# Performance work log

Measured on AMD Instinct MI355X. Metric: run time of the kernel, lower is better.

Reference implementation:

```python
import jax, jax.numpy as jnp
import numpy as np

N = 40000          # nodes
E = 320000         # edges
IN_DIM = 16
H = 64             # num_hidden
EDGE_DIM = 8
NUM_FILTERS = 2
SCALE = 3
T = 4              # num_layers (time steps)
DC = EDGE_DIM * NUM_FILTERS   # edge_dim_cat = 16
HC = H + DC                   # concat(h, efeat_p) dim
S1 = SCALE - 1


def setup_inputs() -> dict:
    key = jax.random.key(0)
    ks = jax.random.split(key, 24)
    def nrm(k, shape, fan):
        return jax.random.normal(k, shape, dtype=jnp.float32) / np.float32(np.sqrt(fan))
    return {
        "inputs": jax.random.normal(ks[0], (N, IN_DIM), dtype=jnp.float32),
        "e_feats": jax.random.normal(ks[1], (E, EDGE_DIM, T), dtype=jnp.float32),
        "rain0": jax.random.uniform(ks[2], (N, T), dtype=jnp.float32),
        "src": jax.random.randint(ks[3], (E,), 0, N),
        "dst": jax.random.randint(ks[4], (E,), 0, N),
        # embedding (no bias)
        "W_emb": nrm(ks[5], (IN_DIM, H), IN_DIM),
        # ST_EIConvSPGRAD (IN) layers, one per scale step: edge MLP split into per-source terms
        "Win_hs": nrm(ks[6], (S1, H, H), 2 * H + EDGE_DIM + 1),
        "Win_hd": nrm(ks[7], (S1, H, H), 2 * H + EDGE_DIM + 1),
        "Win_e": nrm(ks[8], (S1, EDGE_DIM, H), 2 * H + EDGE_DIM + 1),
        "Win_r": nrm(ks[9], (S1, H), 2 * H + EDGE_DIM + 1),
        # ST_EIConvProp (PROP) layers (edge-feature propagation, out_on=False)
        "Wp_hs": nrm(ks[10], (S1, H, DC), 2 * H + DC + 1),
        "Wp_hd": nrm(ks[11], (S1, H, DC), 2 * H + DC + 1),
        "Wp_e": nrm(ks[12], (S1, DC, DC), 2 * H + DC + 1),
        "Wp_r": nrm(ks[13], (S1, DC), 2 * H + DC + 1),
        # ST_EIConvProp OUT layer (out_on=True) on concatenated node features
        "Wo_hs": nrm(ks[14], (HC, H), 2 * HC + EDGE_DIM + 1),
        "Wo_hd": nrm(ks[15], (HC, H), 2 * HC + EDGE_DIM + 1),
        "Wo_e": nrm(ks[16], (EDGE_DIM, H), 2 * HC + EDGE_DIM + 1),
        "Wo_r": nrm(ks[17], (H,), 2 * HC + EDGE_DIM + 1),
        "W_rain": nrm(ks[18], (H,), H),
    }


def reference(inputs, e_feats, rain0, src, dst,
              W_emb, Win_hs, Win_hd, Win_e, Win_r,
              Wp_hs, Wp_hd, Wp_e, Wp_r,
              Wo_hs, Wo_hd, Wo_e, Wo_r, W_rain):
    relu = jax.nn.relu
    agg = lambda m: jax.ops.segment_sum(m, dst, num_segments=N)

    def in_layer(s, h, ef, rain):
        # per-edge message: MLP over [h_src, h_dst, efeat, rain_src], split matmuls avoid concat
        m = relu(h[src] @ Win_hs[s] + h[dst] @ Win_hd[s]
                 + ef @ Win_e[s] + rain[src, None] * Win_r[s][None, :])
        return relu(agg(m))                      # [N, H]

    def prop_layer(s, h, ef, rain):
        # ef is edge-level [E, DC] on first call, node-level [N, DC] thereafter (gather at src)
        ef_e = ef if ef.shape[0] == E else ef[src]
        m = relu(h[src] @ Wp_hs[s] + h[dst] @ Wp_hd[s]
                 + ef_e @ Wp_e[s] + rain[src, None] * Wp_r[s][None, :])
        return agg(m)                            # [N, DC]

    def out_layer(h_out, ef, rain):
        m = relu(h_out[src] @ Wo_hs + h_out[dst] @ Wo_hd
                 + ef @ Wo_e + rain[src, None] * Wo_r[None, :])
        h_new = relu(agg(m))                     # [N, H]
        rain_out = h_new @ W_rain                # [N]
        return rain_out, h_new

    def step(h, ef_t, rain_t, first):
        for s in range(S1):
            h = in_layer(s, h, ef_t, rain_t)
        ef_exp = jnp.tile(ef_t, (1, NUM_FILTERS))        # [E, DC]
        p = prop_layer(0, h, ef_exp, rain_t)
        # faithful quirk: first time step re-applies PROP[0] (range starts at 0);
        # later steps start at 1
        rng = range(S1) if first else range(1, S1)
        for s in rng:
            p = prop_layer(s, h, p, rain_t)
        h_out = jnp.concatenate([h, p], axis=1)          # [N, HC]
        rain_m, h = out_layer(h_out, ef_t, rain_t)
        return rain_m, h

    h = inputs @ W_emb                                   # [N, H]
    rains = []
    for t in range(T):
        rain_m, h = step(h, e_feats[:, :, t], rain0[:, t], first=(t == 0))
        rains.append(rain_m)
    return jnp.stack(rains, axis=1)                      # [N, T]
```

## Files before the change

kernel.cpp:

```cpp
#include <hip/hip_runtime.h>

#define NN 40000
#define NE 320000
#define TT 4
#define SCAN_CHUNK 1024
#define NBLK_SCAN ((NN + SCAN_CHUNK - 1) / SCAN_CHUNK)

typedef float vf4 __attribute__((ext_vector_type(4)));

__device__ __forceinline__ float bcastf(float v, int k) {
    return __builtin_bit_cast(float, __builtin_amdgcn_readlane(__builtin_bit_cast(int, v), k));
}
__device__ __forceinline__ int bcasti(int v, int k) {
    return __builtin_amdgcn_readlane(v, k);
}

__global__ void emb_kernel(const float* __restrict__ x, const float* __restrict__ W,
                           float* __restrict__ h) {
    int i = blockIdx.x * blockDim.x + threadIdx.x;
    if (i >= NN * 64) return;
    int n = i >> 6, j = i & 63;
    float acc = 0.f;
#pragma unroll
    for (int k = 0; k < 16; ++k) acc = fmaf(x[n * 16 + k], W[k * 64 + j], acc);
    h[i] = acc;
}

__global__ void wfold_kernel(const float* __restrict__ We, float* __restrict__ Wf) {
    int i = threadIdx.x;
    if (i < 128) Wf[i] = We[i] + We[i + 128];
}

__global__ void hist_kernel(const int* __restrict__ dst, int* __restrict__ deg) {
    int e = blockIdx.x * blockDim.x + threadIdx.x;
    if (e < NE) atomicAdd(&deg[dst[e]], 1);
}

__global__ void scan1_kernel(const int* __restrict__ deg, int* __restrict__ bsum) {
    __shared__ int sdata[256];
    int b = blockIdx.x, t = threadIdx.x;
    int base = b * SCAN_CHUNK;
    int sum = 0;
    for (int i = t; i < SCAN_CHUNK; i += 256) {
        int idx = base + i;
        sum += (idx < NN) ? deg[idx] : 0;
    }
    sdata[t] = sum;
    __syncthreads();
    for (int off = 128; off > 0; off >>= 1) {
        if (t < off) sdata[t] += sdata[t + off];
        __syncthreads();
    }
    if (t == 0) bsum[b] = sdata[0];
}

__global__ void scan2_kernel(const int* __restrict__ bsum, int* __restrict__ boff,
                             int* __restrict__ rowptr) {
    if (threadIdx.x == 0) {
        int acc = 0;
        for (int i = 0; i < NBLK_SCAN; ++i) {
            boff[i] = acc;
            acc += bsum[i];
        }
        rowptr[NN] = NE;
    }
}

__global__ void scan3_kernel(const int* __restrict__ deg, const int* __restrict__ boff,
                             int* __restrict__ rowptr) {
    __shared__ int ss[256];
    int b = blockIdx.x, t = threadIdx.x;
    int base = b * SCAN_CHUNK + t * 4;
    int v[4], s = 0;
#pragma unroll
    for (int q = 0; q < 4; ++q) {
        int idx = base + q;
        v[q] = (idx < NN) ? deg[idx] : 0;
        s += v[q];
    }
    ss[t] = s;
    __syncthreads();
    for (int off = 1; off < 256; off <<= 1) {
        int add = (t >= off) ? ss[t - off] : 0;
        __syncthreads();
        ss[t] += add;
        __syncthreads();
    }
    int excl = boff[b] + ss[t] - s;
#pragma unroll
    for (int q = 0; q < 4; ++q) {
        int idx = base + q;
        if (idx < NN) rowptr[idx] = excl;
        excl += v[q];
    }
}

__global__ void scatter_kernel(const int* __restrict__ src, const int* __restrict__ dst,
                               int* __restrict__ cursor, int* __restrict__ perm,
                               int* __restrict__ srcp) {
    int e = blockIdx.x * blockDim.x + threadIdx.x;
    if (e >= NE) return;
    int d = dst[e];
    int pos = atomicAdd(&cursor[d], 1);
    perm[pos] = e;
    srcp[pos] = src[e];
}

__global__ void efperm_all_kernel(const float* __restrict__ ef, const int* __restrict__ perm,
                                  float* __restrict__ out) {
    int pos = blockIdx.x * blockDim.x + threadIdx.x;
    if (pos >= NE) return;
    int e = perm[pos];
    const float4* e4 = reinterpret_cast<const float4*>(ef) + (size_t)e * 8;
#pragma unroll
    for (int k = 0; k < 8; ++k) {
        float4 v = e4[k];
        out[0 * (size_t)NE * 8 + pos * 8 + k] = v.x;
        out[1 * (size_t)NE * 8 + pos * 8 + k] = v.y;
        out[2 * (size_t)NE * 8 + pos * 8 + k] = v.z;
        out[3 * (size_t)NE * 8 + pos * 8 + k] = v.w;
    }
}

__global__ void efperm_one_kernel(const float* __restrict__ ef, const int* __restrict__ perm,
                                  int t, float* __restrict__ out) {
    int i = blockIdx.x * blockDim.x + threadIdx.x;
    if (i >= NE * 8) return;
    int pos = i >> 3, k = i & 7;
    int e = perm[pos];
    out[i] = ef[((size_t)e * 8 + k) * 4 + t];
}

__global__ __launch_bounds__(256) void node_ab_kernel(
    const float* __restrict__ X1, int relu1,
    const float* __restrict__ X2, int d2,
    const float* __restrict__ Whs, const float* __restrict__ Whd,
    const float* __restrict__ rain, const float* __restrict__ Wr,
    float* __restrict__ A, float* __restrict__ B) {
    extern __shared__ float sW[];
    const int dtot = 64 + d2;
    float* sWs = sW;
    float* sWd = sW + (dtot << 6);
    for (int i = threadIdx.x; i < (dtot << 6); i += 256) {
        sWs[i] = Whs[i];
        sWd[i] = Whd[i];
    }
    __syncthreads();
    const int lane = threadIdx.x & 63;
    const int wid = (blockIdx.x << 2) + (threadIdx.x >> 6);
    const int n0 = wid << 3;
    const float wr = Wr[lane];
    float xv[8], aa[8], bb[8];
#pragma unroll
    for (int p = 0; p < 8; ++p) {
        float x = __builtin_nontemporal_load(&X1[(n0 + p) * 64 + lane]);
        xv[p] = relu1 ? fmaxf(x, 0.f) : x;
        aa[p] = rain[(n0 + p) * TT] * wr;
        bb[p] = 0.f;
    }
#pragma unroll 16
    for (int k = 0; k < 64; ++k) {
        float ws = sWs[(k << 6) + lane];
        float wd = sWd[(k << 6) + lane];
#pragma unroll
        for (int p = 0; p < 8; ++p) {
            float xk = bcastf(xv[p], k);
            aa[p] = fmaf(xk, ws, aa[p]);
            bb[p] = fmaf(xk, wd, bb[p]);
        }
    }
    if (d2) {
#pragma unroll
        for (int p = 0; p < 8; ++p) xv[p] = X2[(n0 + p) * 16 + (lane & 15)];
#pragma unroll
        for (int k = 0; k < 16; ++k) {
            float ws = sWs[((64 + k) << 6) + lane];
            float wd = sWd[((64 + k) << 6) + lane];
#pragma unroll
            for (int p = 0; p < 8; ++p) {
                float xk = bcastf(xv[p], k);
                aa[p] = fmaf(xk, ws, aa[p]);
                bb[p] = fmaf(xk, wd, bb[p]);
            }
        }
    }
#pragma unroll
    for (int p = 0; p < 8; ++p) {
        A[(n0 + p) * 64 + lane] = aa[p];
        B[(n0 + p) * 64 + lane] = bb[p];
    }
}

__global__ __launch_bounds__(256) void node_p_kernel(
    const float* __restrict__ X, const float* __restrict__ P, int has_p,
    const float* __restrict__ Whs, const float* __restrict__ Whd,
    const float* __restrict__ We,
    const float* __restrict__ rain, const float* __restrict__ Wr,
    float* __restrict__ Ap, float* __restrict__ Bp) {
    __shared__ float sX[64 * 68];
    __shared__ float sP[64 * 20];
    __shared__ float sWs[1024], sWd[1024], sWe[256];
    for (int i = threadIdx.x; i < 1024; i += 256) {
        sWs[i] = Whs[i];
        sWd[i] = Whd[i];
    }
    sWe[threadIdx.x] = has_p ? We[threadIdx.x] : 0.f;
    const int n0 = blockIdx.x << 6;
    for (int i = threadIdx.x; i < 1024; i += 256) {
        int row = i >> 4, col = (i & 15) << 2;
        const float4 v = *reinterpret_cast<const float4*>(&X[(n0 + row) * 64 + col]);
        float* d = &sX[row * 68 + col];
        d[0] = fmaxf(v.x, 0.f);
        d[1] = fmaxf(v.y, 0.f);
        d[2] = fmaxf(v.z, 0.f);
        d[3] = fmaxf(v.w, 0.f);
    }
    if (has_p) {
        int row = threadIdx.x >> 2, col = (threadIdx.x & 3) << 2;
        const float4 v = *reinterpret_cast<const float4*>(&P[(n0 + row) * 16 + col]);
        float* d = &sP[row * 20 + col];
        d[0] = v.x; d[1] = v.y; d[2] = v.z; d[3] = v.w;
    }
    __syncthreads();
    const int j = threadIdx.x & 15;
    const int nl0 = threadIdx.x >> 4;
    const float wr = Wr[j];
    float a[4], b[4];
#pragma unroll
    for (int q = 0; q < 4; ++q) {
        int n = n0 + nl0 + (q << 4);
        a[q] = rain[n * TT] * wr;
        b[q] = 0.f;
    }
#pragma unroll 8
    for (int k = 0; k < 64; ++k) {
        float wa = sWs[(k << 4) + j];
        float wb = sWd[(k << 4) + j];
#pragma unroll
        for (int q = 0; q < 4; ++q) {
            float x = sX[(nl0 + (q << 4)) * 68 + k];
            a[q] = fmaf(x, wa, a[q]);
            b[q] = fmaf(x, wb, b[q]);
        }
    }
    if (has_p) {
#pragma unroll
        for (int k = 0; k < 16; ++k) {
            float wa = sWe[(k << 4) + j];
#pragma unroll
            for (int q = 0; q < 4; ++q) {
                float x = sP[(nl0 + (q << 4)) * 20 + k];
                a[q] = fmaf(x, wa, a[q]);
            }
        }
    }
#pragma unroll
    for (int q = 0; q < 4; ++q) {
        int n = n0 + nl0 + (q << 4);
        Ap[n * 16 + j] = a[q];
        Bp[n * 16 + j] = b[q];
    }
}

__global__ __launch_bounds__(256) void edge64_csr(
    const float* __restrict__ A, const float* __restrict__ B,
    const float* __restrict__ efp, const float* __restrict__ We,
    const int* __restrict__ rowptr, const int* __restrict__ srcp,
    float* __restrict__ agg, const float* __restrict__ Wrain,
    float* __restrict__ out, int t) {
    const int lane = threadIdx.x & 63;
    const int n = (blockIdx.x << 2) + (threadIdx.x >> 6);
    const float w0 = We[0 * 64 + lane], w1 = We[1 * 64 + lane];
    const float w2 = We[2 * 64 + lane], w3 = We[3 * 64 + lane];
    const float w4 = We[4 * 64 + lane], w5 = We[5 * 64 + lane];
    const float w6 = We[6 * 64 + lane], w7 = We[7 * 64 + lane];
    const int beg = rowptr[n], end = rowptr[n + 1];
    const int deg = end - beg;
    int sv = 0;
    if (beg + lane < NE) sv = srcp[beg + lane];
    const float b = __builtin_nontemporal_load(&B[(size_t)n * 64 + lane]);
    const vf4* ef4 = reinterpret_cast<const vf4*>(efp);
    float acc = 0.f;
    for (int k0 = 0; k0 < deg; k0 += 4) {
        float av[4];
        vf4 f0[4], f1[4];
#pragma unroll
        for (int i = 0; i < 4; ++i) {
            int kk = k0 + i;
            if (kk > deg - 1) kk = deg - 1;
            int s = (kk < 64) ? bcasti(sv, kk) : srcp[beg + kk];
            av[i] = A[(size_t)s * 64 + lane];
            f0[i] = ef4[(size_t)(beg + kk) * 2];
            f1[i] = ef4[(size_t)(beg + kk) * 2 + 1];
        }
#pragma unroll
        for (int i = 0; i < 4; ++i) {
            if (k0 + i < deg) {
                float m = av[i] + b;
                m = fmaf(f0[i].x, w0, m);
                m = fmaf(f0[i].y, w1, m);
                m = fmaf(f0[i].z, w2, m);
                m = fmaf(f0[i].w, w3, m);
                m = fmaf(f1[i].x, w4, m);
                m = fmaf(f1[i].y, w5, m);
                m = fmaf(f1[i].z, w6, m);
                m = fmaf(f1[i].w, w7, m);
                acc += fmaxf(m, 0.f);
            }
        }
    }
    __builtin_nontemporal_store(acc, &agg[(size_t)n * 64 + lane]);
    if (out) {
        float r = fmaxf(acc, 0.f) * Wrain[lane];
#pragma unroll
        for (int off = 32; off > 0; off >>= 1) r += __shfl_down(r, off);
        if (lane == 0) out[n * TT + t] = r;
    }
}

__global__ __launch_bounds__(256) void edge16_csr_ef(
    const float* __restrict__ Ap, const float* __restrict__ Bp,
    const float* __restrict__ efp, const float* __restrict__ Wf,
    const int* __restrict__ rowptr, const int* __restrict__ srcp,
    float* __restrict__ aggp) {
    const int lane = threadIdx.x & 63;
    const int g = lane >> 4, j = lane & 15;
    float w[8];
#pragma unroll
    for (int k = 0; k < 8; ++k) w[k] = Wf[k * 16 + j];
    const int wid = (blockIdx.x * 256 + threadIdx.x) >> 6;
    const int n = (wid << 2) + g;
    const int beg = rowptr[n], end = rowptr[n + 1];
    const float b = __builtin_nontemporal_load(&Bp[n * 16 + j]);
    const vf4* ef4 = reinterpret_cast<const vf4*>(efp);
    float acc = 0.f;
    int s_nxt = (beg + 1 < end) ? srcp[beg + 1] : 0;
    float av = (beg < end) ? Ap[srcp[beg] * 16 + j] : 0.f;
    for (int pos = beg; pos < end; ++pos) {
        float avc = av;
        int s_nn = (pos + 2 < end) ? srcp[pos + 2] : 0;
        if (pos + 1 < end) av = Ap[s_nxt * 16 + j];
        s_nxt = s_nn;
        vf4 f0 = ef4[(size_t)pos * 2];
        vf4 f1 = ef4[(size_t)pos * 2 + 1];
        float m = avc + b;
        m = fmaf(f0.x, w[0], m);
        m = fmaf(f0.y, w[1], m);
        m = fmaf(f0.z, w[2], m);
        m = fmaf(f0.w, w[3], m);
        m = fmaf(f1.x, w[4], m);
        m = fmaf(f1.y, w[5], m);
        m = fmaf(f1.z, w[6], m);
        m = fmaf(f1.w, w[7], m);
        acc += fmaxf(m, 0.f);
    }
    aggp[n * 16 + j] = acc;
}

__global__ __launch_bounds__(256) void edge16_csr_pe(
    const float* __restrict__ Ap, const float* __restrict__ Bp,
    const int* __restrict__ rowptr, const int* __restrict__ srcp,
    float* __restrict__ aggp) {
    const int lane = threadIdx.x & 63;
    const int g = lane >> 4, j = lane & 15;
    const int wid = (blockIdx.x * 256 + threadIdx.x) >> 6;
    const int n = (wid << 2) + g;
    const int beg = rowptr[n], end = rowptr[n + 1];
    const float b = __builtin_nontemporal_load(&Bp[n * 16 + j]);
    float acc = 0.f;
    int s_nxt = (beg + 1 < end) ? srcp[beg + 1] : 0;
    float av = (beg < end) ? Ap[srcp[beg] * 16 + j] : 0.f;
    for (int pos = beg; pos < end; ++pos) {
        float avc = av;
        int s_nn = (pos + 2 < end) ? srcp[pos + 2] : 0;
        if (pos + 1 < end) av = Ap[s_nxt * 16 + j];
        s_nxt = s_nn;
        acc += fmaxf(avc + b, 0.f);
    }
    aggp[n * 16 + j] = acc;
}

extern "C" void kernel_launch(void* const* d_in, const int* in_sizes, int n_in,
                              void* d_out, int out_size, void* d_ws, size_t ws_size,
                              hipStream_t stream) {
    (void)in_sizes; (void)n_in; (void)out_size;
    const float* inputs = (const float*)d_in[0];
    const float* e_feats = (const float*)d_in[1];
    const float* rain0 = (const float*)d_in[2];
    const int* src = (const int*)d_in[3];
    const int* dst = (const int*)d_in[4];
    const float* W_emb = (const float*)d_in[5];
    const float* Win_hs = (const float*)d_in[6];
    const float* Win_hd = (const float*)d_in[7];
    const float* Win_e = (const float*)d_in[8];
    const float* Win_r = (const float*)d_in[9];
    const float* Wp_hs = (const float*)d_in[10];
    const float* Wp_hd = (const float*)d_in[11];
    const float* Wp_e = (const float*)d_in[12];
    const float* Wp_r = (const float*)d_in[13];
    const float* Wo_hs = (const float*)d_in[14];
    const float* Wo_hd = (const float*)d_in[15];
    const float* Wo_e = (const float*)d_in[16];
    const float* Wo_r = (const float*)d_in[17];
    const float* W_rain = (const float*)d_in[18];
    float* out = (float*)d_out;

    const size_t NF64 = (size_t)NN * 64;
    const size_t NF16 = (size_t)NN * 16;
    const size_t EF = (size_t)NE * 8;

    const size_t int_bytes = (2 * (size_t)NE + 2 * (size_t)NN + 1 + 128) * 4;
    const size_t need_big = (6 * NF64 + 4 * NF16 + 4 * EF + 128) * 4 + int_bytes;
    const bool big = ws_size >= need_big;

    float* ws = (float*)d_ws;
    float *A, *B, *aggA, *aggB, *aggO, *hemb, *p0, *p1, *Ap, *Bp, *efp, *Wfold;
    if (big) {
        A = ws;    ws += NF64;
        B = ws;    ws += NF64;
        aggA = ws; ws += NF64;
        aggB = ws; ws += NF64;
        aggO = ws; ws += NF64;
        hemb = ws; ws += NF64;
        p0 = ws;   ws += NF16;
        p1 = ws;   ws += NF16;
        Ap = ws;   ws += NF16;
        Bp = ws;   ws += NF16;
        efp = ws;  ws += 4 * EF;
        Wfold = ws; ws += 128;
    } else {
        A = ws;    ws += NF64;
        B = ws;    ws += NF64;
        aggA = ws; ws += NF64;
        aggB = ws; ws += NF64;
        aggO = ws; ws += NF64;
        efp = ws;  ws += EF;
        Wfold = ws; ws += 128;
        hemb = aggO;
        Ap = A;
        Bp = A + NF16;
        p0 = aggA;
        p1 = aggA + NF16;
    }
    int* ip = (int*)ws;
    int* srcp = ip;    ip += NE;
    int* perm = ip;    ip += NE;
    int* rowptr = ip;  ip += NN + 1;
    int* deg = ip;     ip += NN;
    int* bsum = ip;    ip += 64;
    int* boff = ip;    ip += 64;
    int* cursor = deg;

    hipMemsetAsync(deg, 0, NN * sizeof(int), stream);
    hist_kernel<<<(NE + 255) / 256, 256, 0, stream>>>(dst, deg);
    scan1_kernel<<<NBLK_SCAN, 256, 0, stream>>>(deg, bsum);
    scan2_kernel<<<1, 64, 0, stream>>>(bsum, boff, rowptr);
    scan3_kernel<<<NBLK_SCAN, 256, 0, stream>>>(deg, boff, rowptr);
    hipMemcpyAsync(cursor, rowptr, NN * sizeof(int), hipMemcpyDeviceToDevice, stream);
    scatter_kernel<<<(NE + 255) / 256, 256, 0, stream>>>(src, dst, cursor, perm, srcp);
    if (big)
        efperm_all_kernel<<<(NE + 255) / 256, 256, 0, stream>>>(e_feats, perm, efp);

    emb_kernel<<<(NN * 64 + 255) / 256, 256, 0, stream>>>(inputs, W_emb, hemb);
    wfold_kernel<<<1, 128, 0, stream>>>(Wp_e, Wfold);

    for (int t = 0; t < TT; ++t) {
        const float* rain = rain0 + t;
        const float* eft = big ? (efp + (size_t)t * EF) : efp;
        if (!big)
            efperm_one_kernel<<<(NE * 8 + 255) / 256, 256, 0, stream>>>(e_feats, perm, t, efp);

        node_ab_kernel<<<1250, 256, 64 * 64 * 2 * sizeof(float), stream>>>(
            (t == 0) ? hemb : aggO, (t > 0) ? 1 : 0, nullptr, 0,
            Win_hs, Win_hd, rain, Win_r, A, B);
        edge64_csr<<<10000, 256, 0, stream>>>(A, B, eft, Win_e, rowptr, srcp, aggA,
                                              nullptr, nullptr, 0);

        node_ab_kernel<<<1250, 256, 64 * 64 * 2 * sizeof(float), stream>>>(
            aggA, 1, nullptr, 0, Win_hs + 4096, Win_hd + 4096, rain, Win_r + 64, A, B);
        edge64_csr<<<10000, 256, 0, stream>>>(A, B, eft, Win_e + 512, rowptr, srcp, aggB,
                                              nullptr, nullptr, 0);

        node_p_kernel<<<625, 256, 0, stream>>>(aggB, nullptr, 0, Wp_hs, Wp_hd, nullptr,
                                               rain, Wp_r, Ap, Bp);
        edge16_csr_ef<<<2500, 256, 0, stream>>>(Ap, Bp, eft, Wfold, rowptr, srcp, p0);

        float* pc = p0;
        float* pn = p1;
        for (int s = (t == 0) ? 0 : 1; s < 2; ++s) {
            node_p_kernel<<<625, 256, 0, stream>>>(aggB, pc, 1, Wp_hs + s * 1024,
                                                   Wp_hd + s * 1024, Wp_e + s * 256,
                                                   rain, Wp_r + s * 16, Ap, Bp);
            edge16_csr_pe<<<2500, 256, 0, stream>>>(Ap, Bp, rowptr, srcp, pn);
            float* tmp = pc; pc = pn; pn = tmp;
        }

        node_ab_kernel<<<1250, 256, 80 * 64 * 2 * sizeof(float), stream>>>(
            aggB, 1, pc, 16, Wo_hs, Wo_hd, rain, Wo_r, A, B);
        edge64_csr<<<10000, 256, 0, stream>>>(A, B, eft, Wo_e, rowptr, srcp, aggO,
                                              W_rain, out, t);
    }
}
```

Before: 1.077 ms.

## Precompute both PROP layers' node projections once and add small pe16 kernel

The node-side hs/hd projections of aggB for both PROP layers are now computed in one node_p_all kernel, since aggB stays the same across PROP steps. Each later PROP step then only runs a small 16x16 matvec (pe16_kernel) that adds p@Wp_e to the precomputed A term. This removes repeated 64-wide matmuls over all nodes and the reload of X for every PROP step. The edge64 loop is also unrolled to 8 edges per batch and nontemporal load/store hints are dropped. These cost extra workspace buffers and more registers.

```diff
diff --git a/kernel.cpp b/kernel.cpp
--- a/kernel.cpp
+++ b/kernel.cpp
@@ -153,7 +153,7 @@
     float xv[8], aa[8], bb[8];
 #pragma unroll
     for (int p = 0; p < 8; ++p) {
-        float x = __builtin_nontemporal_load(&X1[(n0 + p) * 64 + lane]);
+        float x = X1[(n0 + p) * 64 + lane];
         xv[p] = relu1 ? fmaxf(x, 0.f) : x;
         aa[p] = rain[(n0 + p) * TT] * wr;
         bb[p] = 0.f;
@@ -191,20 +191,20 @@
     }
 }
 
-__global__ __launch_bounds__(256) void node_p_kernel(
-    const float* __restrict__ X, const float* __restrict__ P, int has_p,
+__global__ __launch_bounds__(256) void node_p_all(
+    const float* __restrict__ X,
     const float* __restrict__ Whs, const float* __restrict__ Whd,
-    const float* __restrict__ We,
     const float* __restrict__ rain, const float* __restrict__ Wr,
-    float* __restrict__ Ap, float* __restrict__ Bp) {
+    float* __restrict__ Ap0, float* __restrict__ Bp0,
+    float* __restrict__ Ap1, float* __restrict__ Bp1) {
     __shared__ float sX[64 * 68];
-    __shared__ float sP[64 * 20];
-    __shared__ float sWs[1024], sWd[1024], sWe[256];
+    __shared__ float sW[4][1024];
     for (int i = threadIdx.x; i < 1024; i += 256) {
-        sWs[i] = Whs[i];
-        sWd[i] = Whd[i];
-    }
-    sWe[threadIdx.x] = has_p ? We[threadIdx.x] : 0.f;
+        sW[0][i] = Whs[i];
+        sW[1][i] = Whd[i];
+        sW[2][i] = Whs[1024 + i];
+        sW[3][i] = Whd[1024 + i];
+    }
     const int n0 = blockIdx.x << 6;
     for (int i = threadIdx.x; i < 1024; i += 256) {
         int row = i >> 4, col = (i & 15) << 2;
@@ -215,51 +215,54 @@
         d[2] = fmaxf(v.z, 0.f);
         d[3] = fmaxf(v.w, 0.f);
     }
-    if (has_p) {
-        int row = threadIdx.x >> 2, col = (threadIdx.x & 3) << 2;
-        const float4 v = *reinterpret_cast<const float4*>(&P[(n0 + row) * 16 + col]);
-        float* d = &sP[row * 20 + col];
-        d[0] = v.x; d[1] = v.y; d[2] = v.z; d[3] = v.w;
-    }
     __syncthreads();
     const int j = threadIdx.x & 15;
     const int nl0 = threadIdx.x >> 4;
-    const float wr = Wr[j];
-    float a[4], b[4];
+    const float wr0 = Wr[j], wr1 = Wr[16 + j];
+    float a0[4], b0[4], a1[4], b1[4];
+#pragma unroll
+    for (int q = 0; q < 4; ++q) {
+        float rn = rain[(n0 + nl0 + (q << 4)) * TT];
+        a0[q] = rn * wr0;
+        a1[q] = rn * wr1;
+        b0[q] = 0.f;
+        b1[q] = 0.f;
+    }
+#pragma unroll 4
+    for (int k = 0; k < 64; ++k) {
+        float wa0 = sW[0][(k << 4) + j], wb0 = sW[1][(k << 4) + j];
+        float wa1 = sW[2][(k << 4) + j], wb1 = sW[3][(k << 4) + j];
+#pragma unroll
+        for (int q = 0; q < 4; ++q) {
+            float x = sX[(nl0 + (q << 4)) * 68 + k];
+            a0[q] = fmaf(x, wa0, a0[q]);
+            b0[q] = fmaf(x, wb0, b0[q]);
+            a1[q] = fmaf(x, wa1, a1[q]);
+            b1[q] = fmaf(x, wb1, b1[q]);
+        }
+    }
 #pragma unroll
     for (int q = 0; q < 4; ++q) {
         int n = n0 + nl0 + (q << 4);
-        a[q] = rain[n * TT] * wr;
-        b[q] = 0.f;
-    }
-#pragma unroll 8
-    for (int k = 0; k < 64; ++k) {
-        float wa = sWs[(k << 4) + j];
-        float wb = sWd[(k << 4) + j];
-#pragma unroll
-        for (int q = 0; q < 4; ++q) {
-            float x = sX[(nl0 + (q << 4)) * 68 + k];
-            a[q] = fmaf(x, wa, a[q]);
-            b[q] = fmaf(x, wb, b[q]);
-        }
-    }
-    if (has_p) {
-#pragma unroll
-        for (int k = 0; k < 16; ++k) {
-            float wa = sWe[(k << 4) + j];
-#pragma unroll
-            for (int q = 0; q < 4; ++q) {
-                float x = sP[(nl0 + (q << 4)) * 20 + k];
-                a[q] = fmaf(x, wa, a[q]);
-            }
-        }
-    }
-#pragma unroll
-    for (int q = 0; q < 4; ++q) {
-        int n = n0 + nl0 + (q << 4);
-        Ap[n * 16 + j] = a[q];
-        Bp[n * 16 + j] = b[q];
-    }
+        Ap0[n * 16 + j] = a0[q];
+        Bp0[n * 16 + j] = b0[q];
+        Ap1[n * 16 + j] = a1[q];
+        Bp1[n * 16 + j] = b1[q];
+    }
+}
+
+__global__ __launch_bounds__(256) void pe16_kernel(
+    const float* __restrict__ p, const float* __restrict__ We,
+    const float* __restrict__ Apb, float* __restrict__ PeS) {
+    __shared__ float sW[256];
+    sW[threadIdx.x] = We[threadIdx.x];
+    __syncthreads();
+    int i = blockIdx.x * 256 + threadIdx.x;
+    int n = i >> 4, j = i & 15;
+    float acc = Apb[i];
+#pragma unroll
+    for (int k = 0; k < 16; ++k) acc = fmaf(p[n * 16 + k], sW[k * 16 + j], acc);
+    PeS[i] = acc;
 }
 
 __global__ __launch_bounds__(256) void edge64_csr(
@@ -270,10 +273,10 @@
     float* __restrict__ out, int t) {
     const int lane = threadIdx.x & 63;
     const int n = (blockIdx.x << 2) + (threadIdx.x >> 6);
-    const float w0 = We[0 * 64 + lane], w1 = We[1 * 64 + lane];
-    const float w2 = We[2 * 64 + lane], w3 = We[3 * 64 + lane];
-    const float w4 = We[4 * 64 + lane], w5 = We[5 * 64 + lane];
-    const float w6 = We[6 * 64 + lane], w7 = We[7 * 64 + lane];
+    const float w0 = We[lane], w1 = We[64 + lane];
+    const float w2 = We[128 + lane], w3 = We[192 + lane];
+    const float w4 = We[256 + lane], w5 = We[320 + lane];
+    const float w6 = We[384 + lane], w7 = We[448 + lane];
     const int beg = rowptr[n], end = rowptr[n + 1];
     const int deg = end - beg;
     int sv = 0;
@@ -281,11 +284,11 @@
     const float b = __builtin_nontemporal_load(&B[(size_t)n * 64 + lane]);
     const vf4* ef4 = reinterpret_cast<const vf4*>(efp);
     float acc = 0.f;
-    for (int k0 = 0; k0 < deg; k0 += 4) {
-        float av[4];
-        vf4 f0[4], f1[4];
-#pragma unroll
-        for (int i = 0; i < 4; ++i) {
+    for (int k0 = 0; k0 < deg; k0 += 8) {
+        float av[8];
+        vf4 f0[8], f1[8];
+#pragma unroll
+        for (int i = 0; i < 8; ++i) {
             int kk = k0 + i;
             if (kk > deg - 1) kk = deg - 1;
             int s = (kk < 64) ? bcasti(sv, kk) : srcp[beg + kk];
@@ -294,7 +297,7 @@
             f1[i] = ef4[(size_t)(beg + kk) * 2 + 1];
         }
 #pragma unroll
-        for (int i = 0; i < 4; ++i) {
+        for (int i = 0; i < 8; ++i) {
             if (k0 + i < deg) {
                 float m = av[i] + b;
                 m = fmaf(f0[i].x, w0, m);
@@ -309,7 +312,7 @@
             }
         }
     }
-    __builtin_nontemporal_store(acc, &agg[(size_t)n * 64 + lane]);
+    agg[(size_t)n * 64 + lane] = acc;
     if (out) {
         float r = fmaxf(acc, 0.f) * Wrain[lane];
 #pragma unroll
@@ -331,7 +334,7 @@
     const int wid = (blockIdx.x * 256 + threadIdx.x) >> 6;
     const int n = (wid << 2) + g;
     const int beg = rowptr[n], end = rowptr[n + 1];
-    const float b = __builtin_nontemporal_load(&Bp[n * 16 + j]);
+    const float b = Bp[n * 16 + j];
     const vf4* ef4 = reinterpret_cast<const vf4*>(efp);
     float acc = 0.f;
     int s_nxt = (beg + 1 < end) ? srcp[beg + 1] : 0;
@@ -358,7 +361,7 @@
 }
 
 __global__ __launch_bounds__(256) void edge16_csr_pe(
-    const float* __restrict__ Ap, const float* __restrict__ Bp,
+    const float* __restrict__ PeS, const float* __restrict__ Bp,
     const int* __restrict__ rowptr, const int* __restrict__ srcp,
     float* __restrict__ aggp) {
     const int lane = threadIdx.x & 63;
@@ -366,14 +369,14 @@
     const int wid = (blockIdx.x * 256 + threadIdx.x) >> 6;
     const int n = (wid << 2) + g;
     const int beg = rowptr[n], end = rowptr[n + 1];
-    const float b = __builtin_nontemporal_load(&Bp[n * 16 + j]);
+    const float b = Bp[n * 16 + j];
     float acc = 0.f;
     int s_nxt = (beg + 1 < end) ? srcp[beg + 1] : 0;
-    float av = (beg < end) ? Ap[srcp[beg] * 16 + j] : 0.f;
+    float av = (beg < end) ? PeS[srcp[beg] * 16 + j] : 0.f;
     for (int pos = beg; pos < end; ++pos) {
         float avc = av;
         int s_nn = (pos + 2 < end) ? srcp[pos + 2] : 0;
-        if (pos + 1 < end) av = Ap[s_nxt * 16 + j];
+        if (pos + 1 < end) av = PeS[s_nxt * 16 + j];
         s_nxt = s_nn;
         acc += fmaxf(avc + b, 0.f);
     }
@@ -410,11 +413,12 @@
     const size_t EF = (size_t)NE * 8;
 
     const size_t int_bytes = (2 * (size_t)NE + 2 * (size_t)NN + 1 + 128) * 4;
-    const size_t need_big = (6 * NF64 + 4 * NF16 + 4 * EF + 128) * 4 + int_bytes;
+    const size_t need_big = (6 * NF64 + 7 * NF16 + 4 * EF + 128) * 4 + int_bytes;
     const bool big = ws_size >= need_big;
 
     float* ws = (float*)d_ws;
-    float *A, *B, *aggA, *aggB, *aggO, *hemb, *p0, *p1, *Ap, *Bp, *efp, *Wfold;
+    float *A, *B, *aggA, *aggB, *aggO, *hemb, *p0, *p1;
+    float *Ap0, *Bp0, *Ap1, *Bp1, *PeS, *efp, *Wfold;
     if (big) {
         A = ws;    ws += NF64;
         B = ws;    ws += NF64;
@@ -424,8 +428,11 @@
         hemb = ws; ws += NF64;
         p0 = ws;   ws += NF16;
         p1 = ws;   ws += NF16;
-        Ap = ws;   ws += NF16;
-        Bp = ws;   ws += NF16;
+        Ap0 = ws;  ws += NF16;
+        Bp0 = ws;  ws += NF16;
+        Ap1 = ws;  ws += NF16;
+        Bp1 = ws;  ws += NF16;
+        PeS = ws;  ws += NF16;
         efp = ws;  ws += 4 * EF;
         Wfold = ws; ws += 128;
     } else {
@@ -437,8 +444,11 @@
         efp = ws;  ws += EF;
         Wfold = ws; ws += 128;
         hemb = aggO;
-        Ap = A;
-        Bp = A + NF16;
+        Ap0 = A;
+        Bp0 = A + NF16;
+        Ap1 = A + 2 * NF16;
+        Bp1 = A + 3 * NF16;
+        PeS = B;
         p0 = aggA;
         p1 = aggA + NF16;
     }
@@ -481,17 +491,17 @@
         edge64_csr<<<10000, 256, 0, stream>>>(A, B, eft, Win_e + 512, rowptr, srcp, aggB,
                                               nullptr, nullptr, 0);
 
-        node_p_kernel<<<625, 256, 0, stream>>>(aggB, nullptr, 0, Wp_hs, Wp_hd, nullptr,
-                                               rain, Wp_r, Ap, Bp);
-        edge16_csr_ef<<<2500, 256, 0, stream>>>(Ap, Bp, eft, Wfold, rowptr, srcp, p0);
+        node_p_all<<<625, 256, 0, stream>>>(aggB, Wp_hs, Wp_hd, rain, Wp_r,
+                                            Ap0, Bp0, Ap1, Bp1);
+        edge16_csr_ef<<<2500, 256, 0, stream>>>(Ap0, Bp0, eft, Wfold, rowptr, srcp, p0);
 
         float* pc = p0;
         float* pn = p1;
         for (int s = (t == 0) ? 0 : 1; s < 2; ++s) {
-            node_p_kernel<<<625, 256, 0, stream>>>(aggB, pc, 1, Wp_hs + s * 1024,
-                                                   Wp_hd + s * 1024, Wp_e + s * 256,
-                                                   rain, Wp_r + s * 16, Ap, Bp);
-            edge16_csr_pe<<<2500, 256, 0, stream>>>(Ap, Bp, rowptr, srcp, pn);
+            pe16_kernel<<<2500, 256, 0, stream>>>(pc, Wp_e + s * 256,
+                                                  (s == 0) ? Ap0 : Ap1, PeS);
+            edge16_csr_pe<<<2500, 256, 0, stream>>>(PeS, (s == 0) ? Bp0 : Bp1,
+                                                    rowptr, srcp, pn);
             float* tmp = pc; pc = pn; pn = tmp;
         }
 
```

Measured after the change: 1.227 ms. +13.9%, slower.
